# Kernel tuning notes

Hardware: AMD Instinct MI355X
Metric: run time of the kernel (lower is better)

The kernel has to match this reference:

```python
import jax, jax.numpy as jnp
import numpy as np

N, C, T, V, E = 4, 64, 64, 1024, 4096
IN_CH, OUT_CH, H = 256, 512, 8
DH = OUT_CH // H


def _leaky(x):
    return jnp.where(x >= 0, x, 0.01 * x)


def _mlp(x, w1, b1, w2, b2, g, b):
    # Linear -> LeakyReLU -> (dropout: eval identity) -> Linear -> BatchNorm(batch stats) -> LeakyReLU
    h = _leaky(x @ w1 + b1)
    h = h @ w2 + b2
    n, e, f = h.shape
    flat = h.reshape(n * e, f)
    mu = flat.mean(0)
    var = flat.var(0)  # biased variance, as torch BatchNorm uses for normalization
    flat = (flat - mu) * jax.lax.rsqrt(var + 1e-5) * g + b
    return _leaky(flat.reshape(n, e, f))


def _attn(q, k, v, wq, bq, wk, bk, wv, bv, wf, bf):
    # SelfAttention with scale=1: embed dim == OUT_CH, H heads of DH dims
    n, lq, _ = q.shape
    def split(t):
        return t.reshape(n, -1, H, DH).transpose(0, 2, 1, 3)  # (n, H, L, DH)
    Q = split(q @ wq + bq)
    K = split(k @ wk + bk)
    Vv = split(v @ wv + bv)
    scale = jnp.sqrt(jnp.float32(DH))
    att = jax.nn.softmax(jnp.einsum("nhqd,nhkd->nhqk", Q, K) / scale, axis=-1)
    x = jnp.einsum("nhqk,nhkd->nhqd", att, Vv)
    x = x.transpose(0, 2, 1, 3).reshape(n, lq, OUT_CH)
    return x @ wf + bf


def setup_inputs():
    key = jax.random.key(0)
    ks = list(jax.random.split(key, 24))

    def lin(k1, n_in, n_out):
        w = jax.random.normal(k1, (n_in, n_out), jnp.float32) * np.sqrt(2.0 / (n_in + n_out))
        b = jnp.full((n_out,), 0.1, jnp.float32)
        return w, b

    inp = {
        "x1": jax.random.normal(ks[0], (N, C, T, V), jnp.float32),
        "x2": jax.random.normal(ks[1], (N, C, T, V), jnp.float32),
        "encode1": jax.random.uniform(ks[2], (E, V), dtype=jnp.float32),
        "encode2": jax.random.uniform(ks[3], (E, V), dtype=jnp.float32),
    }
    i = 4
    for name in ("mlp", "nlp"):
        inp[name + "_w1"], inp[name + "_b1"] = lin(ks[i], 2 * IN_CH, OUT_CH); i += 1
        inp[name + "_w2"], inp[name + "_b2"] = lin(ks[i], OUT_CH, OUT_CH); i += 1
        inp[name + "_gamma"] = jnp.ones((OUT_CH,), jnp.float32)
        inp[name + "_beta"] = jnp.zeros((OUT_CH,), jnp.float32)
    for name in ("att1", "att2"):
        for p in ("wq", "wk", "wv", "fc"):
            inp[name + "_" + p + "_w"], inp[name + "_" + p + "_b"] = lin(ks[i], OUT_CH, OUT_CH); i += 1
    return inp


def reference(x1, x2, encode1, encode2,
              mlp_w1, mlp_b1, mlp_w2, mlp_b2, mlp_gamma, mlp_beta,
              nlp_w1, nlp_b1, nlp_w2, nlp_b2, nlp_gamma, nlp_beta,
              att1_wq_w, att1_wq_b, att1_wk_w, att1_wk_b, att1_wv_w, att1_wv_b, att1_fc_w, att1_fc_b,
              att2_wq_w, att2_wq_b, att2_wk_w, att2_wk_b, att2_wv_w, att2_wv_b, att2_fc_w, att2_fc_b):
    n, c, t, v = x1.shape

    def prep(x):
        # permute(0,2,3,1).view(N,V,-1) then AdaptiveAvgPool1d(IN_CH) with exact windows
        x = jnp.transpose(x, (0, 2, 3, 1)).reshape(n, v, t * c)
        return x.reshape(n, v, IN_CH, (t * c) // IN_CH).mean(-1)

    x1p = prep(x1)
    x2p = prep(x2)

    def node_enc(x):
        return jnp.concatenate([
            jnp.einsum("ev,nvc->nec", encode1, x),
            jnp.einsum("ev,nvc->nec", encode2, x),
        ], axis=-1)  # (N, E, 2*IN_CH)

    h1 = _mlp(node_enc(x1p), mlp_w1, mlp_b1, mlp_w2, mlp_b2, mlp_gamma, mlp_beta)
    h2 = _mlp(node_enc(x2p), nlp_w1, nlp_b1, nlp_w2, nlp_b2, nlp_gamma, nlp_beta)

    def edge_enc(h):
        r = jnp.einsum("ev,nec->nvc", encode1, h)  # (N, V, OUT_CH)
        return r / r.shape[1]

    e1 = edge_enc(h1)
    e2 = edge_enc(h2)

    a1 = _attn(e2, e1, e1, att1_wq_w, att1_wq_b, att1_wk_w, att1_wk_b, att1_wv_w, att1_wv_b, att1_fc_w, att1_fc_b)
    a2 = _attn(e1, e2, e2, att2_wq_w, att2_wq_b, att2_wk_w, att2_wk_b, att2_wv_w, att2_wv_b, att2_fc_w, att2_fc_b)

    c1 = jnp.concatenate([a1, a2], axis=1)  # (N, 2V, OUT_CH)
    c2 = jnp.concatenate([a2, a1], axis=1)
    A = jax.nn.softmax(jnp.einsum("nic,njc->nij", c1, c2), axis=-1)  # (N, 2V, 2V)
    # normalize_dynamic_digraph: AGCN-style column-degree normalization A @ D^{-1}
    col = A.sum(axis=1, keepdims=True)
    return A * jnp.where(col > 0, 1.0 / col, 0.0)
```

## Files before the change

### kernel.cpp

```cpp
#include <hip/hip_runtime.h>
#include <hip/hip_bf16.h>

#define LEAKY(v) ((v) >= 0.f ? (v) : 0.01f * (v))

typedef __attribute__((ext_vector_type(8))) short short8b;
typedef __attribute__((ext_vector_type(4))) float f32x4;
typedef __attribute__((ext_vector_type(4))) unsigned short us4;

__device__ __forceinline__ unsigned short f2b(float f) {
  unsigned int u = __builtin_bit_cast(unsigned int, f);
  return (unsigned short)((u + 0x7FFFu + ((u >> 16) & 1u)) >> 16);
}
__device__ __forceinline__ float b2f(unsigned short s) {
  return __builtin_bit_cast(float, (unsigned int)s << 16);
}

__device__ __forceinline__ void gload16(const unsigned short* g, unsigned short* l) {
  __builtin_amdgcn_global_load_lds(
      (const __attribute__((address_space(1))) unsigned int*)(g),
      (__attribute__((address_space(3))) unsigned int*)(l), 16, 0, 0);
}

__device__ __forceinline__ void stage64(const unsigned short* g, int ldg,
                                        unsigned short* lds, int lane, int w) {
  const int r8 = lane >> 3;
  const int ce = ((lane & 7) ^ r8) << 3;
  const int r0 = w * 8 + r8;
  gload16(g + (long)r0 * ldg + ce, lds + w * 512);
  gload16(g + (long)(r0 + 32) * ldg + ce, lds + 2048 + w * 512);
}

__device__ __forceinline__ short8b ldsw(const unsigned short* base, int row, int c4) {
  return *(const short8b*)&base[row * 64 + (((c4 ^ (row & 7)) << 3))];
}

__global__ __launch_bounds__(256) void prep_partial(const float* __restrict__ X1,
                                                    const float* __restrict__ X2,
                                                    float* __restrict__ S) {
  const int t = blockIdx.x;
  const int y = blockIdx.y;
  const int z = blockIdx.z;
  const float* X = (z >> 2) ? X2 : X1;
  const int n = z & 3;
  const int tid = threadIdx.x;
  const long base = (((long)n * 64 + y * 4) * 64 + t) * 1024 + tid * 4;
  const float4 a = *(const float4*)&X[base];
  const float4 b = *(const float4*)&X[base + 65536];
  const float4 c = *(const float4*)&X[base + 2 * 65536];
  const float4 d = *(const float4*)&X[base + 3 * 65536];
  float4 o;
  o.x = (a.x + b.x) + (c.x + d.x);
  o.y = (a.y + b.y) + (c.y + d.y);
  o.z = (a.z + b.z) + (c.z + d.z);
  o.w = (a.w + b.w) + (c.w + d.w);
  *(float4*)&S[(((long)z * 16 + y) * 64 + t) * 1024 + tid * 4] = o;
}

__global__ __launch_bounds__(256) void prep_finish(const float* __restrict__ S,
                                                   unsigned short* __restrict__ Pt) {
  const int t = blockIdx.x;
  const int cbi = blockIdx.y;
  const int z = blockIdx.z;
  const int n = z & 3, inp = z >> 2;
  const int tid = threadIdx.x;
  __shared__ unsigned short sacc[64][20];
  const long sb = (((long)z * 16 + cbi * 4) * 64 + t) * 1024 + tid * 4;
  const float4 a = *(const float4*)&S[sb];
  const float4 b = *(const float4*)&S[sb + 65536];
  const float4 c = *(const float4*)&S[sb + 2 * 65536];
  const float4 d = *(const float4*)&S[sb + 3 * 65536];
  float acc[4];
  acc[0] = (a.x + b.x) + (c.x + d.x);
  acc[1] = (a.y + b.y) + (c.y + d.y);
  acc[2] = (a.z + b.z) + (c.z + d.z);
  acc[3] = (a.w + b.w) + (c.w + d.w);
  const int q = tid & 15, vb = tid >> 4;
#pragma unroll
  for (int j = 0; j < 4; ++j)
    sacc[q * 4 + j][vb] = f2b(acc[j] * (1.f / 16.f));
  __syncthreads();
  const int vvv = tid >> 2, iq = tid & 3;
  const us4 o = *(const us4*)&sacc[vvv][iq * 4];
  *(us4*)&Pt[(long)inp * (1L << 20) + (long)n * 262144 +
             (long)(vvv * 4 + cbi) * 1024 + t * 16 + iq * 4] = o;
}

__global__ __launch_bounds__(256) void transpose_f2b(
    const float* __restrict__ in, unsigned short* __restrict__ out, int R, int C) {
  __shared__ float t[64][65];
  const int c0 = blockIdx.x * 64, r0 = blockIdx.y * 64;
  const int tid = threadIdx.x;
#pragma unroll
  for (int it = 0; it < 4; ++it) {
    int idx = tid + it * 256;
    int r = idx >> 4, c4 = (idx & 15) * 4;
    float4 v = *(const float4*)&in[(long)(r0 + r) * C + c0 + c4];
    t[c4 + 0][r] = v.x; t[c4 + 1][r] = v.y;
    t[c4 + 2][r] = v.z; t[c4 + 3][r] = v.w;
  }
  __syncthreads();
#pragma unroll
  for (int it = 0; it < 4; ++it) {
    int idx = tid + it * 256;
    int c = idx >> 4, r4 = (idx & 15) * 4;
    us4 o;
    o[0] = f2b(t[c][r4 + 0]); o[1] = f2b(t[c][r4 + 1]);
    o[2] = f2b(t[c][r4 + 2]); o[3] = f2b(t[c][r4 + 3]);
    *(us4*)&out[(long)(c0 + c) * R + r0 + r4] = o;
  }
}

struct WPtrs { const float* p[12]; float sc[12]; };
__global__ __launch_bounds__(256) void wtrans(WPtrs wp, unsigned short* __restrict__ out) {
  const float* in = wp.p[blockIdx.z];
  const float s = wp.sc[blockIdx.z];
  unsigned short* ob = out + (long)blockIdx.z * 262144;
  __shared__ float t[64][65];
  const int c0 = blockIdx.x * 64, r0 = blockIdx.y * 64;
  const int tid = threadIdx.x;
#pragma unroll
  for (int it = 0; it < 4; ++it) {
    int idx = tid + it * 256;
    int r = idx >> 4, c4 = (idx & 15) * 4;
    float4 v = *(const float4*)&in[(long)(r0 + r) * 512 + c0 + c4];
    t[c4 + 0][r] = v.x; t[c4 + 1][r] = v.y;
    t[c4 + 2][r] = v.z; t[c4 + 3][r] = v.w;
  }
  __syncthreads();
#pragma unroll
  for (int it = 0; it < 4; ++it) {
    int idx = tid + it * 256;
    int c = idx >> 4, r4 = (idx & 15) * 4;
    us4 o;
    o[0] = f2b(t[c][r4 + 0] * s); o[1] = f2b(t[c][r4 + 1] * s);
    o[2] = f2b(t[c][r4 + 2] * s); o[3] = f2b(t[c][r4 + 3] * s);
    *(us4*)&ob[(long)(c0 + c) * 512 + r0 + r4] = o;
  }
}

__global__ __launch_bounds__(256) void convert2_f2b(const float* __restrict__ i1,
                                                    const float* __restrict__ i2,
                                                    unsigned short* __restrict__ out) {
  const float* in = blockIdx.z ? i2 : i1;
  unsigned short* o = out + (long)blockIdx.z * (4L << 20);
  long i = (long)blockIdx.x * 256 + threadIdx.x;
  float4 v = ((const float4*)in)[i];
  us4 q;
  q[0] = f2b(v.x); q[1] = f2b(v.y); q[2] = f2b(v.z); q[3] = f2b(v.w);
  ((us4*)o)[i] = q;
}

__global__ __launch_bounds__(256) void addcvt(const float* __restrict__ P0,
                                              const float* __restrict__ P1,
                                              unsigned short* __restrict__ out,
                                              float alpha) {
  const long i = ((long)blockIdx.x * 256 + threadIdx.x) * 4;
  const float4 a = *(const float4*)&P0[i];
  const float4 b = *(const float4*)&P1[i];
  us4 o;
  o[0] = f2b((a.x + b.x) * alpha);
  o[1] = f2b((a.y + b.y) * alpha);
  o[2] = f2b((a.z + b.z) * alpha);
  o[3] = f2b((a.w + b.w) * alpha);
  *(us4*)&out[i] = o;
}

struct GDesc { const unsigned short* A; const unsigned short* B; long coff;
               const float* bias; int mode; float bscale; };
struct GDescs { GDesc d[16]; };

template <int ACT, int CMODE, int KSPLIT>
__global__ __launch_bounds__(256) void gemm_z(
    GDescs ga, void* __restrict__ Cv, int K, int lda, int ldb, int ldc,
    long sC2, float alpha) {
  const int bz = blockIdx.z;
  const int s = (KSPLIT > 1) ? (bz % KSPLIT) : 0;
  const int zb = (KSPLIT > 1) ? (bz / KSPLIT) : bz;
  const GDesc g = ga.d[zb];
  const unsigned short* Ab = g.A + (long)s * K;
  const unsigned short* Bb = g.B + (long)s * K;
  const int m0 = blockIdx.y * 128, n0 = blockIdx.x * 128;
  const int tid = threadIdx.x;
  const int lane = tid & 63, w = tid >> 6;
  const int wr = (w >> 1) * 64, wc = (w & 1) * 64;
  __shared__ unsigned short As[128 * 64];
  __shared__ unsigned short Bs[128 * 64];
  f32x4 acc[4][4];
#pragma unroll
  for (int i = 0; i < 4; ++i)
#pragma unroll
    for (int j = 0; j < 4; ++j) acc[i][j] = (f32x4){0.f, 0.f, 0.f, 0.f};
  const int srow = tid >> 3;
  const int scol = (((tid & 7) ^ ((tid >> 3) & 7)) << 3);
  const int rl = lane & 15, lg = lane >> 4, rx = rl & 7;
  for (int k0 = 0; k0 < K; k0 += 64) {
    __syncthreads();
#pragma unroll
    for (int it = 0; it < 4; ++it) {
      gload16(Ab + (long)(m0 + it * 32 + srow) * lda + k0 + scol,
              As + w * 512 + it * 2048);
      gload16(Bb + (long)(n0 + it * 32 + srow) * ldb + k0 + scol,
              Bs + w * 512 + it * 2048);
    }
    __syncthreads();
#pragma unroll
    for (int kk = 0; kk < 2; ++kk) {
      short8b af[4], bfr[4];
#pragma unroll
      for (int m = 0; m < 4; ++m)
        af[m] = *(const short8b*)&As[(wr + m * 16 + rl) * 64 +
                                     ((((kk * 4 + lg) ^ rx)) << 3)];
#pragma unroll
      for (int nn = 0; nn < 4; ++nn)
        bfr[nn] = *(const short8b*)&Bs[(wc + nn * 16 + rl) * 64 +
                                       ((((kk * 4 + lg) ^ rx)) << 3)];
#pragma unroll
      for (int m = 0; m < 4; ++m)
#pragma unroll
        for (int nn = 0; nn < 4; ++nn)
          acc[m][nn] = __builtin_amdgcn_mfma_f32_16x16x32_bf16(
              af[m], bfr[nn], acc[m][nn], 0, 0, 0);
    }
  }
  const int rrow = lg * 4;
  float bv[4];
#pragma unroll
  for (int nn = 0; nn < 4; ++nn)
    bv[nn] = g.bias ? g.bias[n0 + wc + nn * 16 + rl] * g.bscale : 0.f;
  const bool vt_layout = (CMODE == 2) || (CMODE == 4 && g.mode == 2);
  if (CMODE == 2 || CMODE == 4) {
    if (vt_layout) {
#pragma unroll
      for (int m = 0; m < 4; ++m)
#pragma unroll
        for (int nn = 0; nn < 4; ++nn) {
          const int row = m0 + wr + m * 16 + rrow;
          const int col = n0 + wc + nn * 16 + rl;
          us4 o;
#pragma unroll
          for (int r = 0; r < 4; ++r) {
            float v = alpha * acc[m][nn][r] + bv[nn];
            if (ACT == 1) v = LEAKY(v);
            o[r] = f2b(v);
          }
          const long off = g.coff + (long)(row >> 10) * 524288 +
                           (long)col * 1024 + (row & 1023);
          *(us4*)&((unsigned short*)Cv)[off] = o;
        }
    } else {
#pragma unroll
      for (int m = 0; m < 4; ++m)
#pragma unroll
        for (int nn = 0; nn < 4; ++nn)
#pragma unroll
          for (int r = 0; r < 4; ++r) {
            float v = alpha * acc[m][nn][r] + bv[nn];
            if (ACT == 1) v = LEAKY(v);
            const long off = g.coff +
                             (long)(m0 + wr + m * 16 + rrow + r) * ldc + n0 +
                             wc + nn * 16 + rl;
            ((unsigned short*)Cv)[off] = f2b(v);
          }
    }
  } else if (CMODE == 3) {
#pragma unroll
    for (int m = 0; m < 4; ++m)
#pragma unroll
      for (int nn = 0; nn < 4; ++nn) {
        const int row = m0 + wr + m * 16 + rrow;
        const int col = n0 + wc + nn * 16 + rl;
        us4 o;
#pragma unroll
        for (int r = 0; r < 4; ++r) {
          float v = alpha * acc[m][nn][r] + bv[nn];
          if (ACT == 1) v = LEAKY(v);
          o[r] = f2b(v);
        }
        *(us4*)&((unsigned short*)Cv)[g.coff + (long)col * ldc + row] = o;
      }
  } else {
#pragma unroll
    for (int m = 0; m < 4; ++m)
#pragma unroll
      for (int nn = 0; nn < 4; ++nn)
#pragma unroll
        for (int r = 0; r < 4; ++r) {
          float v = alpha * acc[m][nn][r] + bv[nn];
          if (ACT == 1) v = LEAKY(v);
          long off = g.coff + (long)s * sC2 +
                     (long)(m0 + wr + m * 16 + rrow + r) * ldc + n0 + wc +
                     nn * 16 + rl;
          if (CMODE == 1)
            ((unsigned short*)Cv)[off] = f2b(v);
          else
            ((float*)Cv)[off] = v;
        }
  }
}

__global__ __launch_bounds__(256) void bn_fused(
    unsigned short* __restrict__ X,
    const float* __restrict__ g1, const float* __restrict__ be1,
    const float* __restrict__ g2, const float* __restrict__ be2) {
  const int f = blockIdx.x;
  const int z = blockIdx.z;
  unsigned short* p = X + (long)z * (8L << 20) + (long)f * 16384;
  const int tid = threadIdx.x;
  us4 v[16];
  float s = 0.f, q = 0.f;
#pragma unroll
  for (int k = 0; k < 16; ++k) {
    v[k] = *(const us4*)&p[(k * 256 + tid) * 4];
#pragma unroll
    for (int j = 0; j < 4; ++j) {
      const float x = b2f(v[k][j]);
      s += x; q += x * x;
    }
  }
#pragma unroll
  for (int mask = 1; mask < 64; mask <<= 1) {
    s += __shfl_xor(s, mask, 64);
    q += __shfl_xor(q, mask, 64);
  }
  __shared__ float rs[8];
  const int wv = tid >> 6;
  if ((tid & 63) == 0) { rs[wv] = s; rs[4 + wv] = q; }
  __syncthreads();
  s = rs[0] + rs[1] + rs[2] + rs[3];
  q = rs[4] + rs[5] + rs[6] + rs[7];
  const float mu = s * (1.f / 16384.f);
  const float var = q * (1.f / 16384.f) - mu * mu;
  const float gg = (z ? g2 : g1)[f];
  const float bb0 = (z ? be2 : be1)[f];
  const float rstd = rsqrtf(var + 1e-5f) * gg;
  const float bb = bb0 - mu * rstd;
#pragma unroll
  for (int k = 0; k < 16; ++k) {
    us4 o;
#pragma unroll
    for (int j = 0; j < 4; ++j) {
      const float y = b2f(v[k][j]) * rstd + bb;
      o[j] = f2b(LEAKY(y));
    }
    *(us4*)&p[(k * 256 + tid) * 4] = o;
  }
}

__global__ __launch_bounds__(256) void attn_mfma(
    const unsigned short* __restrict__ Q, const unsigned short* __restrict__ K,
    const unsigned short* __restrict__ Vt, unsigned short* __restrict__ O) {
  const int qb = blockIdx.x, h = blockIdx.y;
  const int n = blockIdx.z & 3, sel = blockIdx.z >> 2;
  Q += (long)sel * 4194304;
  K += (long)sel * 4194304;
  Vt += (long)sel * 2097152;
  O += (long)sel * 2097152;
  const int tid = threadIdx.x;
  const int lane = tid & 63, w = tid >> 6;
  const int rl = lane & 15, lg = lane >> 4;
  __shared__ unsigned short Qs[4096];
  __shared__ unsigned short Ks[4096];
  __shared__ unsigned short Vs[4096];
  __shared__ unsigned short Ps[4096];
  stage64(Q + ((long)n * 1024 + qb * 64) * 512 + h * 64, 512, Qs, lane, w);
  float l_r = 0.f;
  f32x4 po[4];
#pragma unroll
  for (int i = 0; i < 4; ++i) po[i] = (f32x4){0.f, 0.f, 0.f, 0.f};
  const unsigned short* Kg0 = K + ((long)n * 1024) * 512 + h * 64;
  const unsigned short* Vg0 = Vt + (long)n * 524288 + (long)(h * 64) * 1024;
  for (int kt = 0; kt < 16; ++kt) {
    __syncthreads();
    stage64(Kg0 + (long)(kt * 64) * 512, 512, Ks, lane, w);
    stage64(Vg0 + kt * 64, 1024, Vs, lane, w);
    __syncthreads();
    f32x4 sa[4];
#pragma unroll
    for (int i = 0; i < 4; ++i) sa[i] = (f32x4){0.f, 0.f, 0.f, 0.f};
#pragma unroll
    for (int kk = 0; kk < 2; ++kk) {
      const short8b qf = ldsw(Qs, w * 16 + rl, 4 * kk + lg);
#pragma unroll
      for (int mt = 0; mt < 4; ++mt) {
        const short8b kf = ldsw(Ks, mt * 16 + rl, 4 * kk + lg);
        sa[mt] = __builtin_amdgcn_mfma_f32_16x16x32_bf16(kf, qf, sa[mt], 0, 0, 0);
      }
    }
    float ps = 0.f;
    const int q = w * 16 + rl;
#pragma unroll
    for (int mt = 0; mt < 4; ++mt) {
      us4 o;
#pragma unroll
      for (int r = 0; r < 4; ++r) {
        const float p = exp2f(sa[mt][r]);
        ps += p;
        o[r] = f2b(p);
      }
      const int c16 = (4 * mt + lg) >> 1;
      *(us4*)&Ps[q * 64 + ((c16 ^ (q & 7)) << 3) + ((lg & 1) << 2)] = o;
    }
    ps += __shfl_xor(ps, 16, 64);
    ps += __shfl_xor(ps, 32, 64);
    l_r += ps;
#pragma unroll
    for (int kk = 0; kk < 2; ++kk) {
      const short8b pf = ldsw(Ps, w * 16 + rl, 4 * kk + lg);
#pragma unroll
      for (int nt = 0; nt < 4; ++nt) {
        const short8b vf = ldsw(Vs, nt * 16 + rl, 4 * kk + lg);
        po[nt] = __builtin_amdgcn_mfma_f32_16x16x32_bf16(pf, vf, po[nt], 0, 0, 0);
      }
    }
  }
  float invr[4];
#pragma unroll
  for (int r = 0; r < 4; ++r) invr[r] = 1.f / __shfl(l_r, lg * 4 + r, 64);
  const long ob = ((long)n * 1024 + qb * 64 + w * 16) * 512 + h * 64;
#pragma unroll
  for (int nt = 0; nt < 4; ++nt)
#pragma unroll
    for (int r = 0; r < 4; ++r)
      O[ob + (long)(lg * 4 + r) * 512 + nt * 16 + rl] = f2b(po[nt][r] * invr[r]);
}

__global__ __launch_bounds__(256) void softmax_cs(const float* __restrict__ D,
                                                  float* __restrict__ RS,
                                                  float* __restrict__ CS) {
  __shared__ float colacc[2048];
  __shared__ float red[8];
  const int tid = threadIdx.x;
  const int wv = tid >> 6, ln = tid & 63;
#pragma unroll
  for (int k = 0; k < 8; ++k) colacc[tid + k * 256] = 0.f;
  __syncthreads();
  const int r0 = blockIdx.x * 8;
  const int n = r0 >> 11;
  for (int rr = 0; rr < 8; ++rr) {
    const float* p = D + (long)(r0 + rr) * 2048;
    float v[8];
    float mx = -1e30f;
#pragma unroll
    for (int k = 0; k < 8; ++k) {
      v[k] = p[tid + k * 256];
      mx = fmaxf(mx, v[k]);
    }
#pragma unroll
    for (int mask = 1; mask < 64; mask <<= 1) mx = fmaxf(mx, __shfl_xor(mx, mask, 64));
    if (ln == 0) red[wv] = mx;
    __syncthreads();
    mx = fmaxf(fmaxf(red[0], red[1]), fmaxf(red[2], red[3]));
    float sum = 0.f;
#pragma unroll
    for (int k = 0; k < 8; ++k) {
      v[k] = __expf(v[k] - mx);
      sum += v[k];
    }
#pragma unroll
    for (int mask = 1; mask < 64; mask <<= 1) sum += __shfl_xor(sum, mask, 64);
    if (ln == 0) red[4 + wv] = sum;
    __syncthreads();
    sum = red[4] + red[5] + red[6] + red[7];
    const float inv = 1.f / sum;
    if (tid == 0) {
      RS[(r0 + rr) * 2] = mx;
      RS[(r0 + rr) * 2 + 1] = inv;
    }
#pragma unroll
    for (int k = 0; k < 8; ++k) colacc[tid + k * 256] += v[k] * inv;
    __syncthreads();
  }
#pragma unroll
  for (int k = 0; k < 8; ++k)
    atomicAdd(&CS[n * 2048 + tid + k * 256], colacc[tid + k * 256]);
}

__global__ __launch_bounds__(256) void final_scale(float* __restrict__ D,
                                                   const float* __restrict__ RS,
                                                   const float* __restrict__ CS) {
  const long i = ((long)blockIdx.x * 256 + threadIdx.x) * 4;
  const long row = i >> 11;
  const int n = (int)(row >> 11);
  const int j = (int)(i & 2047);
  const float mx = RS[row * 2];
  const float inv = RS[row * 2 + 1];
  float4 v = *(float4*)&D[i];
  const float* c = &CS[n * 2048 + j];
  v.x = __expf(v.x - mx) * inv * (c[0] > 0.f ? 1.f / c[0] : 0.f);
  v.y = __expf(v.y - mx) * inv * (c[1] > 0.f ? 1.f / c[1] : 0.f);
  v.z = __expf(v.z - mx) * inv * (c[2] > 0.f ? 1.f / c[2] : 0.f);
  v.w = __expf(v.w - mx) * inv * (c[3] > 0.f ? 1.f / c[3] : 0.f);
  *(float4*)&D[i] = v;
}

extern "C" void kernel_launch(void* const* d_in, const int* in_sizes, int n_in,
                              void* d_out, int out_size, void* d_ws,
                              size_t ws_size, hipStream_t stream) {
  const float* x1 = (const float*)d_in[0];
  const float* x2 = (const float*)d_in[1];
  const float* enc1 = (const float*)d_in[2];
  const float* enc2 = (const float*)d_in[3];
  const float* mlp_b1 = (const float*)d_in[5];
  const float* mlp_b2 = (const float*)d_in[7];
  const float* mlp_g = (const float*)d_in[8];
  const float* mlp_be = (const float*)d_in[9];
  const float* nlp_b1 = (const float*)d_in[11];
  const float* nlp_b2 = (const float*)d_in[13];
  const float* nlp_g = (const float*)d_in[14];
  const float* nlp_be = (const float*)d_in[15];
  float* out = (float*)d_out;

  unsigned short* W = (unsigned short*)d_ws;
  const long M1 = 1L << 20;
  const long S = 262144;
  const float K2 = 0.18033688f;
  unsigned short* Pt = W;
  unsigned short* ENC = W + 4 * M1;
  unsigned short* E1T = W + 12 * M1;
  unsigned short* WT = W + 16 * M1;
  unsigned short* NE = W + 20 * M1;
  unsigned short* H1T = W + 20 * M1;
  unsigned short* MID = W + 36 * M1;
  float* Sprep = (float*)(W + 36 * M1);
  float* P0f = (float*)(W + 36 * M1);
  unsigned short* E1 = W + 4 * M1;
  unsigned short* E2 = W + 6 * M1;
  unsigned short* QKV = W + 36 * M1;
  unsigned short* VT = W + 44 * M1;
  unsigned short* AO = W + 48 * M1;
  unsigned short* A1P = W + 8 * M1;
  unsigned short* A2P = W + 10 * M1;
  float* ST = (float*)(W + 56 * M1);
  float* CS = ST + 2048;
  float* RS = CS + 8192;

  const dim3 T(256);
  const long sP = 262144;
  const long sNE = 2097152;
  const long sE = 524288;
  const long sD = 4194304;

  prep_partial<<<dim3(64, 16, 8), T, 0, stream>>>(x1, x2, Sprep);
  prep_finish<<<dim3(64, 4, 8), T, 0, stream>>>(Sprep, Pt);
  convert2_f2b<<<dim3(4096, 1, 2), T, 0, stream>>>(enc1, enc2, ENC);
  transpose_f2b<<<dim3(16, 64), T, 0, stream>>>(enc1, E1T, 4096, 1024);
  WPtrs wp;
  wp.p[0] = (const float*)d_in[4];   wp.sc[0] = 1.f;
  wp.p[1] = (const float*)d_in[6];   wp.sc[1] = 1.f;
  wp.p[2] = (const float*)d_in[10];  wp.sc[2] = 1.f;
  wp.p[3] = (const float*)d_in[12];  wp.sc[3] = 1.f;
  wp.p[4] = (const float*)d_in[16];  wp.sc[4] = K2;
  wp.p[5] = (const float*)d_in[18];  wp.sc[5] = 1.f;
  wp.p[6] = (const float*)d_in[24];  wp.sc[6] = K2;
  wp.p[7] = (const float*)d_in[26];  wp.sc[7] = 1.f;
  wp.p[8] = (const float*)d_in[20];  wp.sc[8] = 1.f;
  wp.p[9] = (const float*)d_in[28];  wp.sc[9] = 1.f;
  wp.p[10] = (const float*)d_in[22]; wp.sc[10] = 1.f;
  wp.p[11] = (const float*)d_in[30]; wp.sc[11] = 1.f;
  wtrans<<<dim3(8, 8, 12), T, 0, stream>>>(wp, WT);

  {
    GDescs g{};
    for (int inp = 0; inp < 2; ++inp)
      for (int pr = 0; pr < 2; ++pr)
        for (int nn = 0; nn < 4; ++nn)
          g.d[inp * 8 + pr * 4 + nn] = {
              ENC + (long)pr * (4 * M1), Pt + (long)inp * M1 + nn * sP,
              (long)inp * (8 * M1) + (long)nn * sNE + pr * 256, nullptr, 0, 1.f};
    gemm_z<0, 1, 1><<<dim3(2, 32, 16), T, 0, stream>>>(g, NE, 1024, 1024,
                                                       1024, 512, 0, 1.f);
  }
  {
    GDescs g{};
    g.d[0] = {NE, WT + 0 * S, 0, mlp_b1, 0, 1.f};
    g.d[1] = {NE + 8 * M1, WT + 2 * S, 8 * M1, nlp_b1, 0, 1.f};
    gemm_z<1, 1, 1><<<dim3(4, 128, 2), T, 0, stream>>>(g, MID, 512, 512, 512,
                                                       512, 0, 1.f);
  }
  {
    GDescs g{};
    g.d[0] = {MID, WT + 1 * S, 0, mlp_b2, 0, 1.f};
    g.d[1] = {MID + 8 * M1, WT + 3 * S, 8 * M1, nlp_b2, 0, 1.f};
    gemm_z<0, 3, 1><<<dim3(4, 128, 2), T, 0, stream>>>(g, H1T, 512, 512, 512,
                                                       16384, 0, 1.f);
  }
  bn_fused<<<dim3(512, 1, 2), T, 0, stream>>>(H1T, mlp_g, mlp_be, nlp_g, nlp_be);

  {
    GDescs g{};
    for (int d = 0; d < 8; ++d)
      g.d[d] = {E1T, H1T + (long)(d >> 2) * (8 * M1) + (d & 3) * 4096,
                (long)d * 524288, nullptr, 0, 1.f};
    gemm_z<0, 0, 2><<<dim3(4, 8, 16), T, 0, stream>>>(g, P0f, 2048, 4096,
                                                      16384, 512, 4194304, 1.f);
  }
  addcvt<<<4096, T, 0, stream>>>(P0f, P0f + 4194304, E1, 1.f / 1024.f);

  {
    GDescs g{};
    g.d[0] = {E2, WT + 4 * S, 0, (const float*)d_in[17], 1, K2};
    g.d[1] = {E1, WT + 5 * S, 2 * M1, (const float*)d_in[19], 1, 1.f};
    g.d[2] = {E1, WT + 6 * S, 4 * M1, (const float*)d_in[25], 1, K2};
    g.d[3] = {E2, WT + 7 * S, 6 * M1, (const float*)d_in[27], 1, 1.f};
    g.d[4] = {E1, WT + 8 * S, 8 * M1, (const float*)d_in[21], 2, 1.f};
    g.d[5] = {E2, WT + 9 * S, 10 * M1, (const float*)d_in[29], 2, 1.f};
    gemm_z<0, 4, 1><<<dim3(4, 32, 6), T, 0, stream>>>(g, QKV, 512, 512, 512,
                                                      512, 0, 1.f);
  }

  attn_mfma<<<dim3(16, 8, 8), T, 0, stream>>>(QKV, QKV + 2 * M1, VT, AO);

  {
    GDescs g{};
    g.d[0] = {AO, WT + 10 * S, 0, (const float*)d_in[23], 0, 1.f};
    g.d[1] = {AO + 2 * M1, WT + 11 * S, 2 * M1, (const float*)d_in[31], 0, 1.f};
    gemm_z<0, 1, 1><<<dim3(4, 32, 2), T, 0, stream>>>(g, A1P, 512, 512, 512,
                                                      512, 0, 1.f);
  }

  {
    GDescs g{};
    for (int q = 0; q < 4; ++q)
      for (int n = 0; n < 4; ++n) {
        const unsigned short* A = (q < 2 ? A1P : A2P) + n * sE;
        const unsigned short* B = ((q == 0 || q == 2) ? A2P : A1P) + n * sE;
        const long coff =
            (long)n * sD + (q & 1) * 1024 + (long)(q >> 1) * 2097152;
        g.d[q * 4 + n] = {A, B, coff, nullptr, 0, 1.f};
      }
    gemm_z<0, 0, 1><<<dim3(8, 8, 16), T, 0, stream>>>(g, out, 512, 512, 512,
                                                      2048, 0, 1.f);
  }

  hipMemsetAsync(CS, 0, 8192 * sizeof(float), stream);
  softmax_cs<<<1024, T, 0, stream>>>(out, RS, CS);
  final_scale<<<16384, T, 0, stream>>>(out, RS, CS);
}
```

Measured before the change: 379.5 us.

## Merge prologue kernels, use 4-way split-K with bf16 partials, hoist Q fragments

```diff
diff --git a/kernel.cpp b/kernel.cpp
--- a/kernel.cpp
+++ b/kernel.cpp
@@ -34,26 +34,89 @@
   return *(const short8b*)&base[row * 64 + (((c4 ^ (row & 7)) << 3))];
 }
 
-__global__ __launch_bounds__(256) void prep_partial(const float* __restrict__ X1,
-                                                    const float* __restrict__ X2,
-                                                    float* __restrict__ S) {
-  const int t = blockIdx.x;
-  const int y = blockIdx.y;
-  const int z = blockIdx.z;
-  const float* X = (z >> 2) ? X2 : X1;
-  const int n = z & 3;
+struct WPtrs { const float* p[12]; float sc[12]; };
+
+__global__ __launch_bounds__(256) void prologue_misc(
+    const float* __restrict__ X1, const float* __restrict__ X2,
+    float* __restrict__ S, const float* __restrict__ enc1,
+    const float* __restrict__ enc2, unsigned short* __restrict__ ENC,
+    unsigned short* __restrict__ E1T, WPtrs wp,
+    unsigned short* __restrict__ WT) {
+  __shared__ float t[64][65];
+  const int b = blockIdx.x;
   const int tid = threadIdx.x;
-  const long base = (((long)n * 64 + y * 4) * 64 + t) * 1024 + tid * 4;
-  const float4 a = *(const float4*)&X[base];
-  const float4 b = *(const float4*)&X[base + 65536];
-  const float4 c = *(const float4*)&X[base + 2 * 65536];
-  const float4 d = *(const float4*)&X[base + 3 * 65536];
-  float4 o;
-  o.x = (a.x + b.x) + (c.x + d.x);
-  o.y = (a.y + b.y) + (c.y + d.y);
-  o.z = (a.z + b.z) + (c.z + d.z);
-  o.w = (a.w + b.w) + (c.w + d.w);
-  *(float4*)&S[(((long)z * 16 + y) * 64 + t) * 1024 + tid * 4] = o;
+  if (b < 8192) {
+    const int tt = b & 63, y = (b >> 6) & 15, z = b >> 10;
+    const float* X = (z >> 2) ? X2 : X1;
+    const int n = z & 3;
+    const long base = (((long)n * 64 + y * 4) * 64 + tt) * 1024 + tid * 4;
+    const float4 a = *(const float4*)&X[base];
+    const float4 bb = *(const float4*)&X[base + 65536];
+    const float4 c = *(const float4*)&X[base + 2 * 65536];
+    const float4 d = *(const float4*)&X[base + 3 * 65536];
+    float4 o;
+    o.x = (a.x + bb.x) + (c.x + d.x);
+    o.y = (a.y + bb.y) + (c.y + d.y);
+    o.z = (a.z + bb.z) + (c.z + d.z);
+    o.w = (a.w + bb.w) + (c.w + d.w);
+    *(float4*)&S[(((long)z * 16 + y) * 64 + tt) * 1024 + tid * 4] = o;
+  } else if (b < 16384) {
+    const int b2 = b - 8192;
+    const int z = b2 >> 12;
+    const float* in = z ? enc2 : enc1;
+    unsigned short* o = ENC + (long)z * (4L << 20);
+    const long i = (long)(b2 & 4095) * 256 + tid;
+    const float4 v = ((const float4*)in)[i];
+    us4 q;
+    q[0] = f2b(v.x); q[1] = f2b(v.y); q[2] = f2b(v.z); q[3] = f2b(v.w);
+    ((us4*)o)[i] = q;
+  } else if (b < 17408) {
+    const int b3 = b - 16384;
+    const int c0 = (b3 & 15) * 64, r0 = (b3 >> 4) * 64;
+#pragma unroll
+    for (int it = 0; it < 4; ++it) {
+      int idx = tid + it * 256;
+      int r = idx >> 4, c4 = (idx & 15) * 4;
+      float4 v = *(const float4*)&enc1[(long)(r0 + r) * 1024 + c0 + c4];
+      t[c4 + 0][r] = v.x; t[c4 + 1][r] = v.y;
+      t[c4 + 2][r] = v.z; t[c4 + 3][r] = v.w;
+    }
+    __syncthreads();
+#pragma unroll
+    for (int it = 0; it < 4; ++it) {
+      int idx = tid + it * 256;
+      int c = idx >> 4, r4 = (idx & 15) * 4;
+      us4 o;
+      o[0] = f2b(t[c][r4 + 0]); o[1] = f2b(t[c][r4 + 1]);
+      o[2] = f2b(t[c][r4 + 2]); o[3] = f2b(t[c][r4 + 3]);
+      *(us4*)&E1T[(long)(c0 + c) * 4096 + r0 + r4] = o;
+    }
+  } else {
+    const int b4 = b - 17408;
+    const int x = b4 & 7, y = (b4 >> 3) & 7, z = b4 >> 6;
+    const float* in = wp.p[z];
+    const float s = wp.sc[z];
+    unsigned short* ob = WT + (long)z * 262144;
+    const int c0 = x * 64, r0 = y * 64;
+#pragma unroll
+    for (int it = 0; it < 4; ++it) {
+      int idx = tid + it * 256;
+      int r = idx >> 4, c4 = (idx & 15) * 4;
+      float4 v = *(const float4*)&in[(long)(r0 + r) * 512 + c0 + c4];
+      t[c4 + 0][r] = v.x; t[c4 + 1][r] = v.y;
+      t[c4 + 2][r] = v.z; t[c4 + 3][r] = v.w;
+    }
+    __syncthreads();
+#pragma unroll
+    for (int it = 0; it < 4; ++it) {
+      int idx = tid + it * 256;
+      int c = idx >> 4, r4 = (idx & 15) * 4;
+      us4 o;
+      o[0] = f2b(t[c][r4 + 0] * s); o[1] = f2b(t[c][r4 + 1] * s);
+      o[2] = f2b(t[c][r4 + 2] * s); o[3] = f2b(t[c][r4 + 3] * s);
+      *(us4*)&ob[(long)(c0 + c) * 512 + r0 + r4] = o;
+    }
+  }
 }
 
 __global__ __launch_bounds__(256) void prep_finish(const float* __restrict__ S,
@@ -85,83 +148,17 @@
              (long)(vvv * 4 + cbi) * 1024 + t * 16 + iq * 4] = o;
 }
 
-__global__ __launch_bounds__(256) void transpose_f2b(
-    const float* __restrict__ in, unsigned short* __restrict__ out, int R, int C) {
-  __shared__ float t[64][65];
-  const int c0 = blockIdx.x * 64, r0 = blockIdx.y * 64;
-  const int tid = threadIdx.x;
-#pragma unroll
-  for (int it = 0; it < 4; ++it) {
-    int idx = tid + it * 256;
-    int r = idx >> 4, c4 = (idx & 15) * 4;
-    float4 v = *(const float4*)&in[(long)(r0 + r) * C + c0 + c4];
-    t[c4 + 0][r] = v.x; t[c4 + 1][r] = v.y;
-    t[c4 + 2][r] = v.z; t[c4 + 3][r] = v.w;
-  }
-  __syncthreads();
-#pragma unroll
-  for (int it = 0; it < 4; ++it) {
-    int idx = tid + it * 256;
-    int c = idx >> 4, r4 = (idx & 15) * 4;
-    us4 o;
-    o[0] = f2b(t[c][r4 + 0]); o[1] = f2b(t[c][r4 + 1]);
-    o[2] = f2b(t[c][r4 + 2]); o[3] = f2b(t[c][r4 + 3]);
-    *(us4*)&out[(long)(c0 + c) * R + r0 + r4] = o;
-  }
-}
-
-struct WPtrs { const float* p[12]; float sc[12]; };
-__global__ __launch_bounds__(256) void wtrans(WPtrs wp, unsigned short* __restrict__ out) {
-  const float* in = wp.p[blockIdx.z];
-  const float s = wp.sc[blockIdx.z];
-  unsigned short* ob = out + (long)blockIdx.z * 262144;
-  __shared__ float t[64][65];
-  const int c0 = blockIdx.x * 64, r0 = blockIdx.y * 64;
-  const int tid = threadIdx.x;
-#pragma unroll
-  for (int it = 0; it < 4; ++it) {
-    int idx = tid + it * 256;
-    int r = idx >> 4, c4 = (idx & 15) * 4;
-    float4 v = *(const float4*)&in[(long)(r0 + r) * 512 + c0 + c4];
-    t[c4 + 0][r] = v.x; t[c4 + 1][r] = v.y;
-    t[c4 + 2][r] = v.z; t[c4 + 3][r] = v.w;
-  }
-  __syncthreads();
-#pragma unroll
-  for (int it = 0; it < 4; ++it) {
-    int idx = tid + it * 256;
-    int c = idx >> 4, r4 = (idx & 15) * 4;
-    us4 o;
-    o[0] = f2b(t[c][r4 + 0] * s); o[1] = f2b(t[c][r4 + 1] * s);
-    o[2] = f2b(t[c][r4 + 2] * s); o[3] = f2b(t[c][r4 + 3] * s);
-    *(us4*)&ob[(long)(c0 + c) * 512 + r0 + r4] = o;
-  }
-}
-
-__global__ __launch_bounds__(256) void convert2_f2b(const float* __restrict__ i1,
-                                                    const float* __restrict__ i2,
-                                                    unsigned short* __restrict__ out) {
-  const float* in = blockIdx.z ? i2 : i1;
-  unsigned short* o = out + (long)blockIdx.z * (4L << 20);
-  long i = (long)blockIdx.x * 256 + threadIdx.x;
-  float4 v = ((const float4*)in)[i];
-  us4 q;
-  q[0] = f2b(v.x); q[1] = f2b(v.y); q[2] = f2b(v.z); q[3] = f2b(v.w);
-  ((us4*)o)[i] = q;
-}
-
-__global__ __launch_bounds__(256) void addcvt(const float* __restrict__ P0,
-                                              const float* __restrict__ P1,
-                                              unsigned short* __restrict__ out,
-                                              float alpha) {
+__global__ __launch_bounds__(256) void addcvt4(const unsigned short* __restrict__ P,
+                                               unsigned short* __restrict__ out) {
   const long i = ((long)blockIdx.x * 256 + threadIdx.x) * 4;
-  const float4 a = *(const float4*)&P0[i];
-  const float4 b = *(const float4*)&P1[i];
+  const us4 a = *(const us4*)&P[i];
+  const us4 b = *(const us4*)&P[i + 4194304];
+  const us4 c = *(const us4*)&P[i + 2 * 4194304];
+  const us4 d = *(const us4*)&P[i + 3 * 4194304];
   us4 o;
-  o[0] = f2b((a.x + b.x) * alpha);
-  o[1] = f2b((a.y + b.y) * alpha);
-  o[2] = f2b((a.z + b.z) * alpha);
-  o[3] = f2b((a.w + b.w) * alpha);
+#pragma unroll
+  for (int j = 0; j < 4; ++j)
+    o[j] = f2b((b2f(a[j]) + b2f(b[j])) + (b2f(c[j]) + b2f(d[j])));
   *(us4*)&out[i] = o;
 }
 
@@ -363,6 +360,10 @@
   __shared__ unsigned short Vs[4096];
   __shared__ unsigned short Ps[4096];
   stage64(Q + ((long)n * 1024 + qb * 64) * 512 + h * 64, 512, Qs, lane, w);
+  __syncthreads();
+  const int q = w * 16 + rl;
+  const short8b qr0 = ldsw(Qs, q, lg);
+  const short8b qr1 = ldsw(Qs, q, 4 + lg);
   float l_r = 0.f;
   f32x4 po[4];
 #pragma unroll
@@ -379,7 +380,7 @@
     for (int i = 0; i < 4; ++i) sa[i] = (f32x4){0.f, 0.f, 0.f, 0.f};
 #pragma unroll
     for (int kk = 0; kk < 2; ++kk) {
-      const short8b qf = ldsw(Qs, w * 16 + rl, 4 * kk + lg);
+      const short8b qf = kk ? qr1 : qr0;
 #pragma unroll
       for (int mt = 0; mt < 4; ++mt) {
         const short8b kf = ldsw(Ks, mt * 16 + rl, 4 * kk + lg);
@@ -387,7 +388,6 @@
       }
     }
     float ps = 0.f;
-    const int q = w * 16 + rl;
 #pragma unroll
     for (int mt = 0; mt < 4; ++mt) {
       us4 o;
@@ -405,7 +405,7 @@
     l_r += ps;
 #pragma unroll
     for (int kk = 0; kk < 2; ++kk) {
-      const short8b pf = ldsw(Ps, w * 16 + rl, 4 * kk + lg);
+      const short8b pf = ldsw(Ps, q, 4 * kk + lg);
 #pragma unroll
       for (int nt = 0; nt < 4; ++nt) {
         const short8b vf = ldsw(Vs, nt * 16 + rl, 4 * kk + lg);
@@ -522,7 +522,7 @@
   unsigned short* H1T = W + 20 * M1;
   unsigned short* MID = W + 36 * M1;
   float* Sprep = (float*)(W + 36 * M1);
-  float* P0f = (float*)(W + 36 * M1);
+  unsigned short* PB = W + 36 * M1;
   unsigned short* E1 = W + 4 * M1;
   unsigned short* E2 = W + 6 * M1;
   unsigned short* QKV = W + 36 * M1;
@@ -540,10 +540,6 @@
   const long sE = 524288;
   const long sD = 4194304;
 
-  prep_partial<<<dim3(64, 16, 8), T, 0, stream>>>(x1, x2, Sprep);
-  prep_finish<<<dim3(64, 4, 8), T, 0, stream>>>(Sprep, Pt);
-  convert2_f2b<<<dim3(4096, 1, 2), T, 0, stream>>>(enc1, enc2, ENC);
-  transpose_f2b<<<dim3(16, 64), T, 0, stream>>>(enc1, E1T, 4096, 1024);
   WPtrs wp;
   wp.p[0] = (const float*)d_in[4];   wp.sc[0] = 1.f;
   wp.p[1] = (const float*)d_in[6];   wp.sc[1] = 1.f;
@@ -557,7 +553,9 @@
   wp.p[9] = (const float*)d_in[28];  wp.sc[9] = 1.f;
   wp.p[10] = (const float*)d_in[22]; wp.sc[10] = 1.f;
   wp.p[11] = (const float*)d_in[30]; wp.sc[11] = 1.f;
-  wtrans<<<dim3(8, 8, 12), T, 0, stream>>>(wp, WT);
+  prologue_misc<<<18176, T, 0, stream>>>(x1, x2, Sprep, enc1, enc2, ENC, E1T,
+                                         wp, WT);
+  prep_finish<<<dim3(64, 4, 8), T, 0, stream>>>(Sprep, Pt);
 
   {
     GDescs g{};
@@ -591,10 +589,11 @@
     for (int d = 0; d < 8; ++d)
       g.d[d] = {E1T, H1T + (long)(d >> 2) * (8 * M1) + (d & 3) * 4096,
                 (long)d * 524288, nullptr, 0, 1.f};
-    gemm_z<0, 0, 2><<<dim3(4, 8, 16), T, 0, stream>>>(g, P0f, 2048, 4096,
-                                                      16384, 512, 4194304, 1.f);
-  }
-  addcvt<<<4096, T, 0, stream>>>(P0f, P0f + 4194304, E1, 1.f / 1024.f);
+    gemm_z<0, 1, 4><<<dim3(4, 8, 32), T, 0, stream>>>(g, PB, 1024, 4096,
+                                                      16384, 512, 4194304,
+                                                      1.f / 1024.f);
+  }
+  addcvt4<<<4096, T, 0, stream>>>(PB, E1);
 
   {
     GDescs g{};
```

After: 378.5 us. About the same (-0.3%).
